# Kernel optimization log

Hardware: AMD Instinct MI355X
Metric: run time of the kernel (lower is better)

Reference implementation:

```python
import jax, jax.numpy as jnp
import numpy as np

N_NODES = 50000
N_EDGES = 640000
N_FEAT = 128
N_HID = 128
N_CLASS = 16
N_GRAPHS = 64


def setup_inputs() -> dict:
    key = jax.random.key(0)
    ks = jax.random.split(key, 16)
    x = jax.random.normal(ks[0], (N_NODES, N_FEAT), dtype=jnp.float32)
    edge_index = jax.random.randint(ks[1], (2, N_EDGES), 0, N_NODES, dtype=jnp.int64)
    batch = jnp.sort(jax.random.randint(ks[2], (N_NODES,), 0, N_GRAPHS, dtype=jnp.int64))
    def lin(k, fin, fout):
        kw, kb = jax.random.split(k)
        W = jax.random.normal(kw, (fin, fout), dtype=jnp.float32) / np.sqrt(fin)
        b = jnp.zeros((fout,), dtype=jnp.float32)
        return W, b
    W0, b0 = lin(ks[3], N_FEAT, N_HID)
    W1, b1 = lin(ks[4], N_HID, N_HID)
    W2, b2 = lin(ks[5], N_HID, N_HID)
    W3, b3 = lin(ks[6], N_HID, N_HID)  # conv_last
    Wlin, blin = lin(ks[7], N_HID, N_CLASS)
    return {"x": x, "edge_index": edge_index, "batch": batch,
            "W0": W0, "b0": b0, "W1": W1, "b1": b1, "W2": W2, "b2": b2,
            "W3": W3, "b3": b3, "Wlin": Wlin, "blin": blin}


def _gcn_norm(edge_index, n_nodes):
    # GCNConv default: add self-loops, symmetric deg^{-1/2} normalization
    loops = jnp.arange(n_nodes, dtype=edge_index.dtype)
    row = jnp.concatenate([edge_index[0], loops])  # source
    col = jnp.concatenate([edge_index[1], loops])  # target
    ones = jnp.ones(row.shape[0], dtype=jnp.float32)
    deg = jax.ops.segment_sum(ones, col, num_segments=n_nodes)
    dinv = jnp.where(deg > 0, jax.lax.rsqrt(deg), 0.0)
    norm = dinv[row] * dinv[col]  # [E + N]
    return row, col, norm


def _gcn_conv(x, row, col, norm, W, b, n_nodes):
    h = x @ W                          # [N, F_out]
    msg = h[row] * norm[:, None]       # gather + scale, [E+N, F_out]
    out = jax.ops.segment_sum(msg, col, num_segments=n_nodes)
    return out + b


def reference(x, edge_index, batch, W0, b0, W1, b1, W2, b2, W3, b3, Wlin, blin):
    n = x.shape[0]
    row, col, norm = _gcn_norm(edge_index, n)
    h = x
    for (W, b) in ((W0, b0), (W1, b1), (W2, b2)):
        h = _gcn_conv(h, row, col, norm, W, b, n)
        # dropout is identity in eval mode
        h = jax.nn.relu(h)
    h = _gcn_conv(h, row, col, norm, W3, b3, n)
    # global mean pool over graphs
    sums = jax.ops.segment_sum(h, batch, num_segments=N_GRAPHS)
    cnts = jax.ops.segment_sum(jnp.ones((n,), dtype=h.dtype), batch, num_segments=N_GRAPHS)
    pooled = sums / jnp.maximum(cnts, 1.0)[:, None]
    logits = pooled @ Wlin + blin
    return jax.nn.softmax(logits, axis=1)
```

## Files before the change

### kernel.cpp

```cpp
#include <hip/hip_runtime.h>
#include <hip/hip_fp16.h>


typedef _Float16 half8 __attribute__((ext_vector_type(8)));
typedef float f32x4 __attribute__((ext_vector_type(4)));

__device__ __forceinline__ int idx_at(const void* p, long long i, int is64) {
  return is64 ? (int)((const long long*)p)[i] : ((const int*)p)[i];
}

__global__ void k_detect(const int* __restrict__ edge, int* __restrict__ flag) {
  if (threadIdx.x == 0 && blockIdx.x == 0) {
    int all0 = 1;
    for (int i = 1; i < 128; i += 2)
      if (edge[i] != 0) { all0 = 0; break; }
    *flag = all0;
  }
}

__global__ void k_count(const void* __restrict__ edge, int E,
                        int* __restrict__ cnt, const int* __restrict__ flag) {
  int e = blockIdx.x * 256 + threadIdx.x;
  int is64 = *flag;
  if (e < E) {
    int c = idx_at(edge, (long long)E + e, is64);
    atomicAdd(&cnt[c], 1);
  }
}

__global__ void k_dinv(const int* __restrict__ cnt, int n, float* __restrict__ dinv) {
  int i = blockIdx.x * 256 + threadIdx.x;
  if (i < n) dinv[i] = rsqrtf((float)(cnt[i] + 1));
}

__global__ void k_scan1(const int* __restrict__ cnt, int* __restrict__ offs,
                        int* __restrict__ bsum, int n) {
  __shared__ int lds[256];
  int i = blockIdx.x * 256 + threadIdx.x;
  int v = (i < n) ? cnt[i] : 0;
  lds[threadIdx.x] = v;
  __syncthreads();
  for (int off = 1; off < 256; off <<= 1) {
    int t = (threadIdx.x >= off) ? lds[threadIdx.x - off] : 0;
    __syncthreads();
    lds[threadIdx.x] += t;
    __syncthreads();
  }
  if (i < n) offs[i] = lds[threadIdx.x] - v;
  if (threadIdx.x == 255) bsum[blockIdx.x] = lds[255];
}

__global__ void k_scan2(int* __restrict__ bsum, int nb) {
  __shared__ int lds[256];
  int v = (threadIdx.x < nb) ? bsum[threadIdx.x] : 0;
  lds[threadIdx.x] = v;
  __syncthreads();
  for (int off = 1; off < 256; off <<= 1) {
    int t = (threadIdx.x >= off) ? lds[threadIdx.x - off] : 0;
    __syncthreads();
    lds[threadIdx.x] += t;
    __syncthreads();
  }
  if (threadIdx.x < nb) bsum[threadIdx.x] = lds[threadIdx.x] - v;
}

__global__ void k_scan3(int* __restrict__ offs, int* __restrict__ cursor,
                        const int* __restrict__ bsum, int n, int E) {
  int i = blockIdx.x * 256 + threadIdx.x;
  if (i < n) {
    int o = offs[i] + bsum[blockIdx.x];
    offs[i] = o;
    cursor[i] = o;
  }
  if (i == 0) offs[n] = E;
}

__global__ void k_fill(const void* __restrict__ edge, int E,
                       const float* __restrict__ dinv, int* __restrict__ cursor,
                       int2* __restrict__ csr_pair, const int* __restrict__ flag) {
  int e = blockIdx.x * 256 + threadIdx.x;
  int is64 = *flag;
  if (e < E) {
    int r = idx_at(edge, e, is64);
    int c = idx_at(edge, (long long)E + e, is64);
    int p = atomicAdd(&cursor[c], 1);
    float nm = dinv[r] * dinv[c];
    csr_pair[p] = int2{r, __float_as_int(nm)};
  }
}

__global__ void k_wprep(const float* __restrict__ W, _Float16* __restrict__ Wp) {
  int t = blockIdx.x * 256 + threadIdx.x;
  if (t < 16384) {
    int k = t >> 7, c = t & 127;
    int cb = c >> 4, cl = c & 15, ks = k >> 5, kk = k & 31;
    int lane = (kk >> 3) * 16 + cl, j = kk & 7;
    Wp[((cb * 4 + ks) * 64 + lane) * 8 + j] = (_Float16)W[t];
  }
}

__global__ __launch_bounds__(256) void k_gemm16(const _Float16* __restrict__ A16,
                                                const float* __restrict__ A32,
                                                const _Float16* __restrict__ Wp,
                                                _Float16* __restrict__ C16, int n) {
  __shared__ float4 Wl[2048];
  int t = threadIdx.x;
  const float4* Wp4 = (const float4*)Wp;
#pragma unroll
  for (int i = 0; i < 8; i++) Wl[t + 256 * i] = Wp4[t + 256 * i];
  __syncthreads();
  int wave = t >> 6, l = t & 63;
  int m = blockIdx.x * 64 + wave * 16;
  int lr = l & 15, lg = l >> 4;
  int arow = m + lr;
  if (arow > n - 1) arow = n - 1;
  half8 a[4];
  if (A16) {
#pragma unroll
    for (int ks = 0; ks < 4; ks++)
      a[ks] = *(const half8*)(A16 + (size_t)arow * 128 + ks * 32 + lg * 8);
  } else {
#pragma unroll
    for (int ks = 0; ks < 4; ks++) {
      const float4* s = (const float4*)(A32 + (size_t)arow * 128 + ks * 32 + lg * 8);
      float4 s0 = s[0], s1 = s[1];
      half8 v;
      v[0] = (_Float16)s0.x; v[1] = (_Float16)s0.y;
      v[2] = (_Float16)s0.z; v[3] = (_Float16)s0.w;
      v[4] = (_Float16)s1.x; v[5] = (_Float16)s1.y;
      v[6] = (_Float16)s1.z; v[7] = (_Float16)s1.w;
      a[ks] = v;
    }
  }
  const half8* WlH = (const half8*)Wl;
  f32x4 acc[8];
#pragma unroll
  for (int cb = 0; cb < 8; cb++) {
    f32x4 c = {0.f, 0.f, 0.f, 0.f};
#pragma unroll
    for (int ks = 0; ks < 4; ks++) {
      half8 bfrag = WlH[(cb * 4 + ks) * 64 + l];
      c = __builtin_amdgcn_mfma_f32_16x16x32_f16(a[ks], bfrag, c, 0, 0, 0);
    }
    acc[cb] = c;
  }
#pragma unroll
  for (int i = 0; i < 4; i++) {
    int r = m + lg * 4 + i;
    if (r < n) {
#pragma unroll
      for (int cb = 0; cb < 8; cb++)
        C16[(size_t)r * 128 + cb * 16 + lr] = (_Float16)acc[cb][i];
    }
  }
}

__device__ __forceinline__ void fma8(float* acc, uint4 r, float w) {
  union { uint4 u; __half2 h[4]; } cv;
  cv.u = r;
#pragma unroll
  for (int q = 0; q < 4; q++) {
    float2 v = __half22float2(cv.h[q]);
    acc[2 * q] += v.x * w;
    acc[2 * q + 1] += v.y * w;
  }
}

__global__ __launch_bounds__(256) void k_agg(const uint4* __restrict__ h16,
                                             const int* __restrict__ offs,
                                             const int2* __restrict__ csr_pair,
                                             const float* __restrict__ dinv,
                                             const float* __restrict__ bias,
                                             uint4* __restrict__ out16,
                                             int n, int relu) {
  int t = threadIdx.x;
  int wave = t >> 6, l = t & 63;
  int g = l >> 4, sl = l & 15;
  int node = blockIdx.x * 16 + wave * 4 + g;
  if (node >= n) return;
  int s = offs[node], e = offs[node + 1];
  float dn = dinv[node];
  float acc[8];
  {
    uint4 r = h16[(size_t)node * 16 + sl];
    union { uint4 u; __half2 h[4]; } cv;
    cv.u = r;
    float w = dn * dn;
#pragma unroll
    for (int q = 0; q < 4; q++) {
      float2 v = __half22float2(cv.h[q]);
      acc[2 * q] = v.x * w;
      acc[2 * q + 1] = v.y * w;
    }
  }
  int i = s;
  for (; i + 4 <= e; i += 4) {
    int2 p0 = csr_pair[i];
    int2 p1 = csr_pair[i + 1];
    int2 p2 = csr_pair[i + 2];
    int2 p3 = csr_pair[i + 3];
    uint4 r0 = h16[(size_t)p0.x * 16 + sl];
    uint4 r1 = h16[(size_t)p1.x * 16 + sl];
    uint4 r2 = h16[(size_t)p2.x * 16 + sl];
    uint4 r3 = h16[(size_t)p3.x * 16 + sl];
    fma8(acc, r0, __int_as_float(p0.y));
    fma8(acc, r1, __int_as_float(p1.y));
    fma8(acc, r2, __int_as_float(p2.y));
    fma8(acc, r3, __int_as_float(p3.y));
  }
  for (; i < e; i++) {
    int2 p = csr_pair[i];
    uint4 r = h16[(size_t)p.x * 16 + sl];
    fma8(acc, r, __int_as_float(p.y));
  }
  if (bias) {
    const float4* b4 = (const float4*)(bias + sl * 8);
    float4 b0 = b4[0], b1 = b4[1];
    acc[0] += b0.x; acc[1] += b0.y; acc[2] += b0.z; acc[3] += b0.w;
    acc[4] += b1.x; acc[5] += b1.y; acc[6] += b1.z; acc[7] += b1.w;
  }
  if (relu) {
#pragma unroll
    for (int q = 0; q < 8; q++) acc[q] = fmaxf(acc[q], 0.f);
  }
  union { uint4 u; __half2 h[4]; } ov;
#pragma unroll
  for (int q = 0; q < 4; q++)
    ov.h[q] = __floats2half2_rn(acc[2 * q], acc[2 * q + 1]);
  out16[(size_t)node * 16 + sl] = ov.u;
}

#define POOL_CH 64
__global__ __launch_bounds__(128) void k_pool_partial(
    const _Float16* __restrict__ h, const void* __restrict__ batch, int n,
    float* __restrict__ sums, float* __restrict__ cnts,
    const int* __restrict__ flag) {
  int start = blockIdx.x * POOL_CH;
  if (start >= n) return;
  int end = start + POOL_CH;
  if (end > n) end = n;
  int f = threadIdx.x;
  int is64 = *flag;
  int g = idx_at(batch, start, is64);
  float acc = 0.f, c = 0.f;
  for (int i = start; i < end; i++) {
    int gi = idx_at(batch, i, is64);
    if (gi != g) {
      atomicAdd(&sums[g * 128 + f], acc);
      if (f == 0) atomicAdd(&cnts[g], c);
      acc = 0.f; c = 0.f; g = gi;
    }
    acc += (float)h[(size_t)i * 128 + f];
    c += 1.f;
  }
  atomicAdd(&sums[g * 128 + f], acc);
  if (f == 0) atomicAdd(&cnts[g], c);
}

__global__ __launch_bounds__(128) void k_final(const float* __restrict__ sums,
                                               const float* __restrict__ cnts,
                                               const float* __restrict__ W3,
                                               const float* __restrict__ b3,
                                               const float* __restrict__ Wlin,
                                               const float* __restrict__ blin,
                                               float* __restrict__ out) {
  __shared__ float p[128];
  __shared__ float t1[128];
  __shared__ float lg[16];
  int g = blockIdx.x;
  int t = threadIdx.x;
  float inv = 1.f / fmaxf(cnts[g], 1.f);
  p[t] = sums[g * 128 + t] * inv;
  __syncthreads();
  float acc = 0.f;
  for (int k = 0; k < 128; k++) acc += p[k] * W3[k * 128 + t];
  t1[t] = acc + b3[t];
  __syncthreads();
  if (t < 16) {
    float a2 = 0.f;
    for (int k = 0; k < 128; k++) a2 += t1[k] * Wlin[k * 16 + t];
    lg[t] = a2 + blin[t];
  }
  __syncthreads();
  if (t < 16) {
    float m = -1e30f;
    for (int j = 0; j < 16; j++) m = fmaxf(m, lg[j]);
    float s = 0.f;
    for (int j = 0; j < 16; j++) s += expf(lg[j] - m);
    out[g * 16 + t] = expf(lg[t] - m) / s;
  }
}

extern "C" void kernel_launch(void* const* d_in, const int* in_sizes, int n_in,
                              void* d_out, int out_size, void* d_ws, size_t ws_size,
                              hipStream_t stream) {
  const float* x = (const float*)d_in[0];
  const void* edge = d_in[1];
  const void* batch = d_in[2];
  const float* W[4] = {(const float*)d_in[3], (const float*)d_in[5],
                       (const float*)d_in[7], (const float*)d_in[9]};
  const float* b[4] = {(const float*)d_in[4], (const float*)d_in[6],
                       (const float*)d_in[8], (const float*)d_in[10]};
  const float* Wlin = (const float*)d_in[11];
  const float* blin = (const float*)d_in[12];
  float* out = (float*)d_out;

  int n = in_sizes[0] / 128;
  int E = in_sizes[1] / 2;
  int ngraphs = out_size / 16;

  char* ws = (char*)d_ws;
  size_t off = 0;
  auto alloc = [&](size_t bytes) -> void* {
    void* p = ws + off;
    off = (off + bytes + 255) & ~(size_t)255;
    return p;
  };
  int* flag = (int*)alloc(4);
  int* cnt = (int*)alloc((size_t)n * 4);
  int* offs = (int*)alloc((size_t)(n + 1) * 4);
  int* cursor = (int*)alloc((size_t)n * 4);
  float* dinv = (float*)alloc((size_t)n * 4);
  int* bsum = (int*)alloc(1024 * 4);
  int2* csr_pair = (int2*)alloc((size_t)E * 8);
  _Float16* Wp0 = (_Float16*)alloc(16384 * 2);
  _Float16* Wp1 = (_Float16*)alloc(16384 * 2);
  _Float16* Wp2 = (_Float16*)alloc(16384 * 2);
  _Float16* hA = (_Float16*)alloc((size_t)n * 128 * 2);
  _Float16* hB = (_Float16*)alloc((size_t)n * 128 * 2);
  float* sums = (float*)alloc((size_t)ngraphs * 128 * 4);
  float* cnts = (float*)alloc((size_t)ngraphs * 4);

  hipMemsetAsync(cnt, 0, (size_t)n * 4, stream);
  hipMemsetAsync(sums, 0, (size_t)ngraphs * 128 * 4, stream);
  hipMemsetAsync(cnts, 0, (size_t)ngraphs * 4, stream);
  k_detect<<<1, 64, 0, stream>>>((const int*)edge, flag);
  k_count<<<(E + 255) / 256, 256, 0, stream>>>(edge, E, cnt, flag);
  k_dinv<<<(n + 255) / 256, 256, 0, stream>>>(cnt, n, dinv);
  int nb = (n + 255) / 256;
  k_scan1<<<nb, 256, 0, stream>>>(cnt, offs, bsum, n);
  k_scan2<<<1, 256, 0, stream>>>(bsum, nb);
  k_scan3<<<nb, 256, 0, stream>>>(offs, cursor, bsum, n, E);
  k_fill<<<(E + 255) / 256, 256, 0, stream>>>(edge, E, dinv, cursor, csr_pair, flag);
  k_wprep<<<64, 256, 0, stream>>>(W[0], Wp0);
  k_wprep<<<64, 256, 0, stream>>>(W[1], Wp1);
  k_wprep<<<64, 256, 0, stream>>>(W[2], Wp2);

  int ngb = (n + 63) / 64;
  int nagg = (n + 15) / 16;
  k_gemm16<<<ngb, 256, 0, stream>>>(nullptr, x, Wp0, hA, n);
  k_agg<<<nagg, 256, 0, stream>>>((const uint4*)hA, offs, csr_pair, dinv,
                                  b[0], (uint4*)hB, n, 1);
  k_gemm16<<<ngb, 256, 0, stream>>>(hB, nullptr, Wp1, hA, n);
  k_agg<<<nagg, 256, 0, stream>>>((const uint4*)hA, offs, csr_pair, dinv,
                                  b[1], (uint4*)hB, n, 1);
  k_gemm16<<<ngb, 256, 0, stream>>>(hB, nullptr, Wp2, hA, n);
  k_agg<<<nagg, 256, 0, stream>>>((const uint4*)hA, offs, csr_pair, dinv,
                                  b[2], (uint4*)hB, n, 1);
  k_agg<<<nagg, 256, 0, stream>>>((const uint4*)hB, offs, csr_pair, dinv,
                                  nullptr, (uint4*)hA, n, 0);
  k_pool_partial<<<(n + POOL_CH - 1) / POOL_CH, 128, 0, stream>>>(hA, batch, n, sums, cnts, flag);
  k_final<<<ngraphs, 128, 0, stream>>>(sums, cnts, W[3], b[3], Wlin, blin, out);
}
```

Before: 264.5 us.

## Factor symmetric normalization into GEMM epilogue and degree-sort aggregation nodes

Moves the per-edge dinv[r]*dinv[c] weight out of the CSR: the source scale is applied in the GEMM epilogue (or in the previous aggregation's output), and the target scale once per node after summing. The CSR now stores only row indices, halving edge-list bytes and turning per-edge FMAs into adds. It also counting-sorts nodes by degree into a permutation so the four nodes sharing a wave have similar edge counts, which reduces divergence. The cost is three extra small preprocessing kernels and one more rounding point in fp16 for the pre-scaled features.

```diff
diff --git a/kernel.cpp b/kernel.cpp
--- a/kernel.cpp
+++ b/kernel.cpp
@@ -76,16 +76,44 @@
 }
 
 __global__ void k_fill(const void* __restrict__ edge, int E,
-                       const float* __restrict__ dinv, int* __restrict__ cursor,
-                       int2* __restrict__ csr_pair, const int* __restrict__ flag) {
+                       int* __restrict__ cursor, int* __restrict__ csr_row,
+                       const int* __restrict__ flag) {
   int e = blockIdx.x * 256 + threadIdx.x;
   int is64 = *flag;
   if (e < E) {
     int r = idx_at(edge, e, is64);
     int c = idx_at(edge, (long long)E + e, is64);
     int p = atomicAdd(&cursor[c], 1);
-    float nm = dinv[r] * dinv[c];
-    csr_pair[p] = int2{r, __float_as_int(nm)};
+    csr_row[p] = r;
+  }
+}
+
+__global__ void k_dhist(const int* __restrict__ cnt, int n, int* __restrict__ dh) {
+  int i = blockIdx.x * 256 + threadIdx.x;
+  if (i < n) atomicAdd(&dh[min(cnt[i], 127)], 1);
+}
+
+__global__ void k_dscan(int* __restrict__ dh) {
+  __shared__ int lds[128];
+  int t = threadIdx.x;
+  int v = dh[t];
+  lds[t] = v;
+  __syncthreads();
+  for (int off = 1; off < 128; off <<= 1) {
+    int u = (t >= off) ? lds[t - off] : 0;
+    __syncthreads();
+    lds[t] += u;
+    __syncthreads();
+  }
+  dh[t] = lds[t] - v;
+}
+
+__global__ void k_dscatter(const int* __restrict__ cnt, int n,
+                           int* __restrict__ dcur, int* __restrict__ perm) {
+  int i = blockIdx.x * 256 + threadIdx.x;
+  if (i < n) {
+    int p = atomicAdd(&dcur[min(cnt[i], 127)], 1);
+    perm[p] = i;
   }
 }
 
@@ -102,6 +130,7 @@
 __global__ __launch_bounds__(256) void k_gemm16(const _Float16* __restrict__ A16,
                                                 const float* __restrict__ A32,
                                                 const _Float16* __restrict__ Wp,
+                                                const float* __restrict__ dinv,
                                                 _Float16* __restrict__ C16, int n) {
   __shared__ float4 Wl[2048];
   int t = threadIdx.x;
@@ -148,71 +177,74 @@
   for (int i = 0; i < 4; i++) {
     int r = m + lg * 4 + i;
     if (r < n) {
+      float sc = dinv[r];
 #pragma unroll
       for (int cb = 0; cb < 8; cb++)
-        C16[(size_t)r * 128 + cb * 16 + lr] = (_Float16)acc[cb][i];
+        C16[(size_t)r * 128 + cb * 16 + lr] = (_Float16)(acc[cb][i] * sc);
     }
   }
 }
 
-__device__ __forceinline__ void fma8(float* acc, uint4 r, float w) {
+__device__ __forceinline__ void add8(float* acc, uint4 r) {
   union { uint4 u; __half2 h[4]; } cv;
   cv.u = r;
 #pragma unroll
   for (int q = 0; q < 4; q++) {
     float2 v = __half22float2(cv.h[q]);
-    acc[2 * q] += v.x * w;
-    acc[2 * q + 1] += v.y * w;
+    acc[2 * q] += v.x;
+    acc[2 * q + 1] += v.y;
   }
 }
 
 __global__ __launch_bounds__(256) void k_agg(const uint4* __restrict__ h16,
                                              const int* __restrict__ offs,
-                                             const int2* __restrict__ csr_pair,
+                                             const int* __restrict__ csr_row,
                                              const float* __restrict__ dinv,
+                                             const int* __restrict__ perm,
                                              const float* __restrict__ bias,
                                              uint4* __restrict__ out16,
-                                             int n, int relu) {
+                                             int n, int relu, int scale_out) {
   int t = threadIdx.x;
   int wave = t >> 6, l = t & 63;
   int g = l >> 4, sl = l & 15;
-  int node = blockIdx.x * 16 + wave * 4 + g;
-  if (node >= n) return;
+  int j = blockIdx.x * 16 + wave * 4 + g;
+  if (j >= n) return;
+  int node = perm[j];
   int s = offs[node], e = offs[node + 1];
-  float dn = dinv[node];
   float acc[8];
   {
     uint4 r = h16[(size_t)node * 16 + sl];
     union { uint4 u; __half2 h[4]; } cv;
     cv.u = r;
-    float w = dn * dn;
 #pragma unroll
     for (int q = 0; q < 4; q++) {
       float2 v = __half22float2(cv.h[q]);
-      acc[2 * q] = v.x * w;
-      acc[2 * q + 1] = v.y * w;
+      acc[2 * q] = v.x;
+      acc[2 * q + 1] = v.y;
     }
   }
   int i = s;
   for (; i + 4 <= e; i += 4) {
-    int2 p0 = csr_pair[i];
-    int2 p1 = csr_pair[i + 1];
-    int2 p2 = csr_pair[i + 2];
-    int2 p3 = csr_pair[i + 3];
-    uint4 r0 = h16[(size_t)p0.x * 16 + sl];
-    uint4 r1 = h16[(size_t)p1.x * 16 + sl];
-    uint4 r2 = h16[(size_t)p2.x * 16 + sl];
-    uint4 r3 = h16[(size_t)p3.x * 16 + sl];
-    fma8(acc, r0, __int_as_float(p0.y));
-    fma8(acc, r1, __int_as_float(p1.y));
-    fma8(acc, r2, __int_as_float(p2.y));
-    fma8(acc, r3, __int_as_float(p3.y));
+    int r0 = csr_row[i];
+    int r1 = csr_row[i + 1];
+    int r2 = csr_row[i + 2];
+    int r3 = csr_row[i + 3];
+    uint4 v0 = h16[(size_t)r0 * 16 + sl];
+    uint4 v1 = h16[(size_t)r1 * 16 + sl];
+    uint4 v2 = h16[(size_t)r2 * 16 + sl];
+    uint4 v3 = h16[(size_t)r3 * 16 + sl];
+    add8(acc, v0);
+    add8(acc, v1);
+    add8(acc, v2);
+    add8(acc, v3);
   }
   for (; i < e; i++) {
-    int2 p = csr_pair[i];
-    uint4 r = h16[(size_t)p.x * 16 + sl];
-    fma8(acc, r, __int_as_float(p.y));
-  }
+    uint4 v = h16[(size_t)csr_row[i] * 16 + sl];
+    add8(acc, v);
+  }
+  float dn = dinv[node];
+#pragma unroll
+  for (int q = 0; q < 8; q++) acc[q] *= dn;
   if (bias) {
     const float4* b4 = (const float4*)(bias + sl * 8);
     float4 b0 = b4[0], b1 = b4[1];
@@ -222,6 +254,10 @@
   if (relu) {
 #pragma unroll
     for (int q = 0; q < 8; q++) acc[q] = fmaxf(acc[q], 0.f);
+  }
+  if (scale_out) {
+#pragma unroll
+    for (int q = 0; q < 8; q++) acc[q] *= dn;
   }
   union { uint4 u; __half2 h[4]; } ov;
 #pragma unroll
@@ -322,7 +358,9 @@
   int* cursor = (int*)alloc((size_t)n * 4);
   float* dinv = (float*)alloc((size_t)n * 4);
   int* bsum = (int*)alloc(1024 * 4);
-  int2* csr_pair = (int2*)alloc((size_t)E * 8);
+  int* dh = (int*)alloc(128 * 4);
+  int* perm = (int*)alloc((size_t)n * 4);
+  int* csr_row = (int*)alloc((size_t)E * 4);
   _Float16* Wp0 = (_Float16*)alloc(16384 * 2);
   _Float16* Wp1 = (_Float16*)alloc(16384 * 2);
   _Float16* Wp2 = (_Float16*)alloc(16384 * 2);
@@ -332,6 +370,7 @@
   float* cnts = (float*)alloc((size_t)ngraphs * 4);
 
   hipMemsetAsync(cnt, 0, (size_t)n * 4, stream);
+  hipMemsetAsync(dh, 0, 128 * 4, stream);
   hipMemsetAsync(sums, 0, (size_t)ngraphs * 128 * 4, stream);
   hipMemsetAsync(cnts, 0, (size_t)ngraphs * 4, stream);
   k_detect<<<1, 64, 0, stream>>>((const int*)edge, flag);
@@ -341,24 +380,27 @@
   k_scan1<<<nb, 256, 0, stream>>>(cnt, offs, bsum, n);
   k_scan2<<<1, 256, 0, stream>>>(bsum, nb);
   k_scan3<<<nb, 256, 0, stream>>>(offs, cursor, bsum, n, E);
-  k_fill<<<(E + 255) / 256, 256, 0, stream>>>(edge, E, dinv, cursor, csr_pair, flag);
+  k_fill<<<(E + 255) / 256, 256, 0, stream>>>(edge, E, cursor, csr_row, flag);
+  k_dhist<<<nb, 256, 0, stream>>>(cnt, n, dh);
+  k_dscan<<<1, 128, 0, stream>>>(dh);
+  k_dscatter<<<nb, 256, 0, stream>>>(cnt, n, dh, perm);
   k_wprep<<<64, 256, 0, stream>>>(W[0], Wp0);
   k_wprep<<<64, 256, 0, stream>>>(W[1], Wp1);
   k_wprep<<<64, 256, 0, stream>>>(W[2], Wp2);
 
   int ngb = (n + 63) / 64;
   int nagg = (n + 15) / 16;
-  k_gemm16<<<ngb, 256, 0, stream>>>(nullptr, x, Wp0, hA, n);
-  k_agg<<<nagg, 256, 0, stream>>>((const uint4*)hA, offs, csr_pair, dinv,
-                                  b[0], (uint4*)hB, n, 1);
-  k_gemm16<<<ngb, 256, 0, stream>>>(hB, nullptr, Wp1, hA, n);
-  k_agg<<<nagg, 256, 0, stream>>>((const uint4*)hA, offs, csr_pair, dinv,
-                                  b[1], (uint4*)hB, n, 1);
-  k_gemm16<<<ngb, 256, 0, stream>>>(hB, nullptr, Wp2, hA, n);
-  k_agg<<<nagg, 256, 0, stream>>>((const uint4*)hA, offs, csr_pair, dinv,
-                                  b[2], (uint4*)hB, n, 1);
-  k_agg<<<nagg, 256, 0, stream>>>((const uint4*)hB, offs, csr_pair, dinv,
-                                  nullptr, (uint4*)hA, n, 0);
+  k_gemm16<<<ngb, 256, 0, stream>>>(nullptr, x, Wp0, dinv, hA, n);
+  k_agg<<<nagg, 256, 0, stream>>>((const uint4*)hA, offs, csr_row, dinv, perm,
+                                  b[0], (uint4*)hB, n, 1, 0);
+  k_gemm16<<<ngb, 256, 0, stream>>>(hB, nullptr, Wp1, dinv, hA, n);
+  k_agg<<<nagg, 256, 0, stream>>>((const uint4*)hA, offs, csr_row, dinv, perm,
+                                  b[1], (uint4*)hB, n, 1, 0);
+  k_gemm16<<<ngb, 256, 0, stream>>>(hB, nullptr, Wp2, dinv, hA, n);
+  k_agg<<<nagg, 256, 0, stream>>>((const uint4*)hA, offs, csr_row, dinv, perm,
+                                  b[2], (uint4*)hB, n, 1, 1);
+  k_agg<<<nagg, 256, 0, stream>>>((const uint4*)hB, offs, csr_row, dinv, perm,
+                                  nullptr, (uint4*)hA, n, 0, 0);
   k_pool_partial<<<(n + POOL_CH - 1) / POOL_CH, 128, 0, stream>>>(hA, batch, n, sums, cnts, flag);
   k_final<<<ngraphs, 128, 0, stream>>>(sums, cnts, W[3], b[3], Wlin, blin, out);
 }
```

Result: slower. 571.9 us (+116.2%).
